# Kernel optimization log

Measured on AMD Instinct MI355X. Metric: run time of the kernel, lower is better.

Reference implementation:

```python
import jax, jax.numpy as jnp
import numpy as np

B, D, H, NS = 64, 2048, 4096, 25  # batch, x_dim (num_links), n_hidden=2*x_dim, n_steps


def setup_inputs() -> dict:
    key = jax.random.key(0)
    ks = jax.random.split(key, 12)
    # binary half-masks per leapfrog step (faithful to _construct_masks with np_seed=1)
    rng = np.random.RandomState(1)
    masks = np.zeros((NS, D), np.float32)
    for i in range(NS):
        idx = rng.permutation(D)[: D // 2]
        masks[i, idx] = 1.0
    # sinusoidal time encoding per step (_construct_time)
    ts = np.stack([
        [np.cos(2 * np.pi * i / NS), np.sin(2 * np.pi * i / NS)] for i in range(NS)
    ]).astype(np.float32)

    def lin(k, shape, fan_in):
        return jax.random.normal(k, shape, jnp.float32) / np.sqrt(fan_in)

    return dict(
        position=jax.random.normal(ks[0], (B, D), jnp.float32),
        momentum_f=jax.random.normal(ks[1], (B, D), jnp.float32),
        momentum_b=jax.random.normal(ks[2], (B, D), jnp.float32),
        u_dir=jax.random.uniform(ks[3], (B,), jnp.float32),
        u_accept=jax.random.uniform(ks[4], (B,), jnp.float32),
        eps=jnp.full((1,), 0.1, jnp.float32),
        masks=jnp.asarray(masks),
        ts=jnp.asarray(ts),
        # stacked params for the two GenericNets: [0]=position_fn, [1]=momentum_fn
        W1=lin(ks[5], (2, D, H), D), W2=lin(ks[6], (2, D, H), D),
        Wt=lin(ks[7], (2, 2, H), 2), b1=jnp.zeros((2, H), jnp.float32),
        Wh=lin(ks[8], (2, H, H), H), bh=jnp.zeros((2, H), jnp.float32),
        Ws=lin(ks[9], (2, H, D), H), bs=jnp.zeros((2, D), jnp.float32),
        cs=jnp.zeros((2, D), jnp.float32),
        Wtr=lin(ks[10], (2, H, D), H), btr=jnp.zeros((2, D), jnp.float32),
        Wq=lin(ks[11], (2, H, D), H), bq=jnp.zeros((2, D), jnp.float32),
        cq=jnp.zeros((2, D), jnp.float32),
    )


def reference(position, momentum_f, momentum_b, u_dir, u_accept, eps, masks, ts,
              W1, W2, Wt, b1, Wh, bh, Ws, bs, cs, Wtr, btr, Wq, bq, cq):
    e = eps[0]
    POS, MOM = 0, 1

    def net(n, a, b, t):
        # GenericNet: two-hidden-layer MLP emitting (scale S, translation T, transformation Q)
        h = jax.nn.relu(a @ W1[n] + b @ W2[n] + t @ Wt[n] + b1[n])
        h = jax.nn.relu(h @ Wh[n] + bh[n])
        S = jnp.tanh(h @ Ws[n] + bs[n]) * jnp.exp(cs[n])
        T = h @ Wtr[n] + btr[n]
        Q = jnp.tanh(h @ Wq[n] + bq[n]) * jnp.exp(cq[n])
        return S, T, Q

    def potential(x):              # U(1) gauge-style action: sum(1 - cos(x))
        return jnp.sum(1.0 - jnp.cos(x), axis=1)

    def grad_potential(x):
        return jnp.sin(x)

    def hamiltonian(x, v):
        return potential(x) + 0.5 * jnp.sum(v * v, axis=1)

    def mom_fwd(pos, mom, t):
        g = grad_potential(pos)
        S, T, Q = net(MOM, pos, g, t)
        sc, tr = 0.5 * e * S, e * Q
        mom = mom * jnp.exp(sc) - 0.5 * e * (jnp.exp(tr) * g - T)
        return mom, jnp.sum(sc, axis=1)

    def pos_fwd(pos, mom, t, m, minv):
        S, T, Q = net(POS, mom, m * pos, t)
        sc, tr = e * S, e * Q
        pos = m * pos + minv * (pos * jnp.exp(sc) + e * (jnp.exp(tr) * mom + T))
        return pos, jnp.sum(minv * sc, axis=1)

    def mom_bwd(pos, mom, t):
        g = grad_potential(pos)
        S, T, Q = net(MOM, pos, g, t)
        sc, tr = -0.5 * e * S, e * Q
        mom = jnp.exp(sc) * (mom + 0.5 * e * (jnp.exp(tr) * g - T))
        return mom, jnp.sum(sc, axis=1)

    def pos_bwd(pos, mom, t, m, minv):
        S, T, Q = net(POS, mom, m * pos, t)
        sc, tr = e * S, e * Q
        pos = m * pos + minv * jnp.exp(sc) * (pos - e * (jnp.exp(tr) * mom + T))
        return pos, jnp.sum(minv * sc, axis=1)

    def step_fwd(carry, xs):
        pos, mom, sld = carry
        m, t = xs
        t = t[None, :]
        minv = 1.0 - m
        mom, ld = mom_fwd(pos, mom, t); sld = sld + ld
        pos, ld = pos_fwd(pos, mom, t, m, minv); sld = sld + ld
        pos, ld = pos_fwd(pos, mom, t, minv, m); sld = sld + ld
        mom, ld = mom_fwd(pos, mom, t); sld = sld + ld
        return (pos, mom, sld), None

    def step_bwd(carry, xs):
        pos, mom, sld = carry
        m, t = xs
        t = t[None, :]
        minv = 1.0 - m
        mom, ld = mom_bwd(pos, mom, t); sld = sld + ld
        pos, ld = pos_bwd(pos, mom, t, minv, m); sld = sld + ld
        pos, ld = pos_bwd(pos, mom, t, m, minv); sld = sld + ld
        mom, ld = mom_bwd(pos, mom, t); sld = sld + ld
        return (pos, mom, sld), None

    zero = jnp.zeros(position.shape[0], position.dtype)
    (pf, mf, sldf), _ = jax.lax.scan(step_fwd, (position, momentum_f, zero), (masks, ts))
    (pb, mb, sldb), _ = jax.lax.scan(step_bwd, (position, momentum_b, zero), (masks[::-1], ts[::-1]))

    def accept_prob(mom0, pos1, mom1, sld):
        d = hamiltonian(position, mom0) - hamiltonian(pos1, mom1) + sld
        p = jnp.exp(jnp.minimum(d, 0.0))
        return jnp.where(jnp.isfinite(p), p, jnp.zeros_like(p))

    apf = accept_prob(momentum_f, pf, mf, sldf)
    apb = accept_prob(momentum_b, pb, mb, sldb)

    fmask = (u_dir > 0.5).astype(position.dtype)
    bmask = 1.0 - fmask
    position_post = fmask[:, None] * pf + bmask[:, None] * pb
    momentum_post = fmask[:, None] * mf + bmask[:, None] * mb
    ap = fmask * apf + bmask * apb
    amask = (ap > u_accept).astype(position.dtype)
    position_out = amask[:, None] * position_post + (1.0 - amask)[:, None] * position
    return position_post, momentum_post, ap, position_out
```

## Files before the change

### kernel.cpp

```cpp
#include <hip/hip_runtime.h>

#define BD   64
#define DD   2048
#define HH   4096
#define NSS  25
#define BBr  128

typedef _Float16 halfx8 __attribute__((ext_vector_type(8)));
typedef float    floatx4 __attribute__((ext_vector_type(4)));

__device__ __forceinline__ unsigned short f2h_bits(float x) {
    union { _Float16 h; unsigned short u; } c;
    c.h = (_Float16)x;
    return c.u;
}

__global__ void init_kernel(const float* __restrict__ position,
                            const float* __restrict__ momf,
                            const float* __restrict__ momb,
                            float* __restrict__ pos, float* __restrict__ mom,
                            float* __restrict__ sld,
                            unsigned short* __restrict__ Abuf) {
    int idx = blockIdx.x * 256 + threadIdx.x;
    int r = idx >> 11, d = idx & 2047;
    float p = position[((r & 63) << 11) + d];
    pos[idx] = p;
    mom[idx] = (r < 64) ? momf[(r << 11) + d] : momb[((r - 64) << 11) + d];
    Abuf[(r << 12) + d]        = f2h_bits(p);
    Abuf[(r << 12) + 2048 + d] = f2h_bits(sinf(p));
    if (idx < BBr) sld[idx] = 0.f;
}

__global__ __launch_bounds__(256) void transpose_cvt_kernel(
        const float* __restrict__ src, int ldi,
        unsigned short* __restrict__ dst, int ldo) {
    __shared__ float tile[32][33];
    const int rb = blockIdx.y * 32;
    const int cb = blockIdx.x * 32;
    const int t  = threadIdx.x;
    const int r  = t >> 3;
    const int c4 = (t & 7) * 4;
    float4 v = *reinterpret_cast<const float4*>(src + (size_t)(rb + r) * ldi + cb + c4);
    tile[r][c4 + 0] = v.x; tile[r][c4 + 1] = v.y;
    tile[r][c4 + 2] = v.z; tile[r][c4 + 3] = v.w;
    __syncthreads();
    union { unsigned short us[4]; uint2 v; } pk;
#pragma unroll
    for (int j = 0; j < 4; ++j) pk.us[j] = f2h_bits(tile[c4 + j][r]);
    *reinterpret_cast<uint2*>(dst + (size_t)(cb + r) * ldo + rb + c4) = pk.v;
}

template <int EPI>
__global__ __launch_bounds__(256) void gemm_bt_kernel(
        const unsigned short* __restrict__ A, int lda, int K,
        const unsigned short* __restrict__ BT,
        void* __restrict__ Cout, int ldc,
        const float* __restrict__ biasp, const float* __restrict__ Wtn,
        const float* __restrict__ ts, int sF, int sB) {
    const int lane = threadIdx.x & 63;
    const int wave = threadIdx.x >> 6;
    const int fl   = lane & 15;
    const int qd   = lane >> 4;
    const int bn   = blockIdx.x * 16;

    const unsigned short* pa0 = A  + (size_t)(wave * 32 + fl) * lda + qd * 8;
    const unsigned short* pa1 = pa0 + (size_t)16 * lda;
    const unsigned short* pb  = BT + (size_t)(bn + fl) * K + qd * 8;

    floatx4 acc0 = {0.f, 0.f, 0.f, 0.f};
    floatx4 acc1 = {0.f, 0.f, 0.f, 0.f};

    for (int k0 = 0; k0 < K; k0 += 128) {
#pragma unroll
        for (int u = 0; u < 4; ++u) {
            halfx8 a0 = *reinterpret_cast<const halfx8*>(pa0 + u * 32);
            halfx8 a1 = *reinterpret_cast<const halfx8*>(pa1 + u * 32);
            halfx8 b  = *reinterpret_cast<const halfx8*>(pb  + u * 32);
            acc0 = __builtin_amdgcn_mfma_f32_16x16x32_f16(a0, b, acc0, 0, 0, 0);
            acc1 = __builtin_amdgcn_mfma_f32_16x16x32_f16(a1, b, acc1, 0, 0, 0);
        }
        pa0 += 128; pa1 += 128; pb += 128;
    }

    const int col = bn + fl;
#pragma unroll
    for (int fn = 0; fn < 2; ++fn) {
        floatx4 a = (fn == 0) ? acc0 : acc1;
        const int row_base = wave * 32 + fn * 16 + qd * 4;
#pragma unroll
        for (int rr = 0; rr < 4; ++rr) {
            int row = row_base + rr;
            float v = a[rr];
            if (EPI == 0) {
                int sidx = (row < 64) ? sF : sB;
                v += biasp[col] + ts[2 * sidx] * Wtn[col] + ts[2 * sidx + 1] * Wtn[HH + col];
                v = fmaxf(v, 0.f);
                ((unsigned short*)Cout)[(size_t)row * ldc + col] = f2h_bits(v);
            } else if (EPI == 1) {
                v = fmaxf(v + biasp[col], 0.f);
                ((unsigned short*)Cout)[(size_t)row * ldc + col] = f2h_bits(v);
            } else {
                ((float*)Cout)[(size_t)row * ldc + col] = v;
            }
        }
    }
}

template <int BMODE, int EPI>
__global__ __launch_bounds__(256) void gemm_kernel(
        const unsigned short* __restrict__ A, int lda, int K,
        const float* __restrict__ Bp0, const float* __restrict__ Bp1,
        const float* __restrict__ Bp2, int ldb,
        void* __restrict__ Cout, int ldc,
        const float* __restrict__ biasp, const float* __restrict__ Wtn,
        const float* __restrict__ ts, int sF, int sB) {
    __shared__ unsigned short As[32][40];
    __shared__ unsigned short Bs[64][40];

    const int tid  = threadIdx.x;
    const int wave = tid >> 6;
    const int lane = tid & 63;
    const int fl   = lane & 15;
    const int qd   = lane >> 4;
    const int bm   = blockIdx.y * 32;
    const int bn   = blockIdx.x * 64;
    const int wm   = (wave >> 1) * 16;
    const int wn   = (wave & 1) * 32;

    const int ar = tid >> 3;
    const int ak = (tid & 7) * 4;
    const int kloc = wave * 8;
    const int bnl  = lane;

    floatx4 acc0 = {0.f, 0.f, 0.f, 0.f};
    floatx4 acc1 = {0.f, 0.f, 0.f, 0.f};

    for (int k0 = 0; k0 < K; k0 += 32) {
        *reinterpret_cast<uint2*>(&As[ar][ak]) =
            *reinterpret_cast<const uint2*>(A + (size_t)(bm + ar) * lda + k0 + ak);

        float fv[8];
        if (BMODE == 0) {
            int kk = k0 + kloc;
            const float* base = (kk < 2048) ? (Bp0 + (size_t)kk * ldb)
                                            : (Bp1 + (size_t)(kk - 2048) * ldb);
            base += bn + bnl;
#pragma unroll
            for (int j = 0; j < 8; ++j) fv[j] = base[(size_t)j * ldb];
        } else if (BMODE == 1) {
            const float* base = Bp0 + (size_t)(k0 + kloc) * ldb + bn + bnl;
#pragma unroll
            for (int j = 0; j < 8; ++j) fv[j] = base[(size_t)j * ldb];
        } else {
            int third = bn >> 11;
            const float* Bsel = (third == 0) ? Bp0 : ((third == 1) ? Bp1 : Bp2);
            const float* base = Bsel + (size_t)(k0 + kloc) * ldb + (bn - (third << 11)) + bnl;
#pragma unroll
            for (int j = 0; j < 8; ++j) fv[j] = base[(size_t)j * ldb];
        }
        union { unsigned short us[8]; uint4 v; } pk;
#pragma unroll
        for (int j = 0; j < 8; ++j) pk.us[j] = f2h_bits(fv[j]);
        *reinterpret_cast<uint4*>(&Bs[bnl][kloc]) = pk.v;

        __syncthreads();

        halfx8 afr = *reinterpret_cast<const halfx8*>(&As[wm + fl][qd * 8]);
        halfx8 bf0 = *reinterpret_cast<const halfx8*>(&Bs[wn + fl][qd * 8]);
        halfx8 bf1 = *reinterpret_cast<const halfx8*>(&Bs[wn + 16 + fl][qd * 8]);
        acc0 = __builtin_amdgcn_mfma_f32_16x16x32_f16(afr, bf0, acc0, 0, 0, 0);
        acc1 = __builtin_amdgcn_mfma_f32_16x16x32_f16(afr, bf1, acc1, 0, 0, 0);

        __syncthreads();
    }

    const int row0 = bm + wm + qd * 4;
#pragma unroll
    for (int fn = 0; fn < 2; ++fn) {
        floatx4 a = (fn == 0) ? acc0 : acc1;
        int col = bn + wn + fn * 16 + fl;
#pragma unroll
        for (int rr = 0; rr < 4; ++rr) {
            int row = row0 + rr;
            float v = a[rr];
            if (EPI == 0) {
                int sidx = (row < 64) ? sF : sB;
                v += biasp[col] + ts[2 * sidx] * Wtn[col] + ts[2 * sidx + 1] * Wtn[HH + col];
                v = fmaxf(v, 0.f);
                ((unsigned short*)Cout)[(size_t)row * ldc + col] = f2h_bits(v);
            } else if (EPI == 1) {
                v = fmaxf(v + biasp[col], 0.f);
                ((unsigned short*)Cout)[(size_t)row * ldc + col] = f2h_bits(v);
            } else {
                ((float*)Cout)[(size_t)row * ldc + col] = v;
            }
        }
    }
}

__device__ __forceinline__ void block_reduce_atomic(float v, float* dst) {
    for (int off = 32; off; off >>= 1) v += __shfl_down(v, off, 64);
    __shared__ float red[4];
    if ((threadIdx.x & 63) == 0) red[threadIdx.x >> 6] = v;
    __syncthreads();
    if (threadIdx.x == 0) atomicAdd(dst, red[0] + red[1] + red[2] + red[3]);
}

__global__ void update_mom_kernel(const float* __restrict__ pos, float* __restrict__ mom,
                                  float* __restrict__ sld, const float* __restrict__ STQ,
                                  const float* __restrict__ bs, const float* __restrict__ cs,
                                  const float* __restrict__ btr, const float* __restrict__ bq,
                                  const float* __restrict__ cq, const float* __restrict__ eps,
                                  const float* __restrict__ masks, int sF, int sB,
                                  int writeNext, unsigned short* __restrict__ Abuf) {
    int r = blockIdx.y;
    int d = blockIdx.x * 256 + threadIdx.x;
    float e = eps[0];
    size_t ro = (size_t)r * 6144;
    float S = tanhf(STQ[ro + d] + bs[d]) * expf(cs[d]);
    float T = STQ[ro + 2048 + d] + btr[d];
    float Q = tanhf(STQ[ro + 4096 + d] + bq[d]) * expf(cq[d]);
    size_t idx = (size_t)r * 2048 + d;
    float p = pos[idx], v = mom[idx];
    float g = sinf(p);
    float tr = e * Q, sc;
    if (r < 64) { sc = 0.5f * e * S;  v = v * expf(sc) - 0.5f * e * (expf(tr) * g - T); }
    else        { sc = -0.5f * e * S; v = expf(sc) * (v + 0.5f * e * (expf(tr) * g - T)); }
    mom[idx] = v;
    if (writeNext) {
        float m2 = (r < 64) ? masks[sF * 2048 + d] : 1.f - masks[sB * 2048 + d];
        Abuf[(r << 12) + d]        = f2h_bits(v);
        Abuf[(r << 12) + 2048 + d] = f2h_bits(m2 * p);
    }
    block_reduce_atomic(sc, sld + r);
}

__global__ void update_pos_kernel(float* __restrict__ pos, const float* __restrict__ mom,
                                  float* __restrict__ sld, const float* __restrict__ STQ,
                                  const float* __restrict__ bs, const float* __restrict__ cs,
                                  const float* __restrict__ btr, const float* __restrict__ bq,
                                  const float* __restrict__ cq, const float* __restrict__ eps,
                                  const float* __restrict__ masks, int sF, int sB, int sub,
                                  unsigned short* __restrict__ Abuf) {
    int r = blockIdx.y;
    int d = blockIdx.x * 256 + threadIdx.x;
    float e = eps[0];
    size_t ro = (size_t)r * 6144;
    float S = tanhf(STQ[ro + d] + bs[d]) * expf(cs[d]);
    float T = STQ[ro + 2048 + d] + btr[d];
    float Q = tanhf(STQ[ro + 4096 + d] + bq[d]) * expf(cq[d]);
    size_t idx = (size_t)r * 2048 + d;
    float p = pos[idx], v = mom[idx];
    float sc = e * S, tr = e * Q;
    float mf = masks[sF * 2048 + d], mb = masks[sB * 2048 + d];
    float pn, ld;
    if (r < 64) {
        float m  = (sub == 2) ? mf : 1.f - mf;
        float mi = 1.f - m;
        pn = m * p + mi * (p * expf(sc) + e * (expf(tr) * v + T));
        ld = mi * sc;
    } else {
        float m  = (sub == 2) ? 1.f - mb : mb;
        float mi = 1.f - m;
        pn = m * p + mi * expf(sc) * (p - e * (expf(tr) * v + T));
        ld = mi * sc;
    }
    pos[idx] = pn;
    if (sub == 2) {
        float m3 = (r < 64) ? 1.f - mf : mb;
        Abuf[(r << 12) + d]        = f2h_bits(v);
        Abuf[(r << 12) + 2048 + d] = f2h_bits(m3 * pn);
    } else {
        Abuf[(r << 12) + d]        = f2h_bits(pn);
        Abuf[(r << 12) + 2048 + d] = f2h_bits(sinf(pn));
    }
    block_reduce_atomic(ld, sld + r);
}

__global__ void accept_kernel(const float* __restrict__ position,
                              const float* __restrict__ momf, const float* __restrict__ momb,
                              const float* __restrict__ pos, const float* __restrict__ mom,
                              const float* __restrict__ sld, float* __restrict__ ap_all) {
    int r = blockIdx.x;
    int rb = r & 63;
    const float* m0 = (r < 64) ? (momf + (size_t)rb * 2048) : (momb + (size_t)rb * 2048);
    float s = 0.f;
    for (int d = threadIdx.x; d < 2048; d += 256) {
        float x0 = position[rb * 2048 + d];
        float v0 = m0[d];
        float x1 = pos[(size_t)r * 2048 + d];
        float v1 = mom[(size_t)r * 2048 + d];
        s += (cosf(x1) - cosf(x0)) + 0.5f * (v0 * v0 - v1 * v1);
    }
    for (int off = 32; off; off >>= 1) s += __shfl_down(s, off, 64);
    __shared__ float red[4];
    if ((threadIdx.x & 63) == 0) red[threadIdx.x >> 6] = s;
    __syncthreads();
    if (threadIdx.x == 0) {
        float dd = red[0] + red[1] + red[2] + red[3] + sld[r];
        float p = isnan(dd) ? 0.f : expf(dd < 0.f ? dd : 0.f);
        if (!isfinite(p)) p = 0.f;
        ap_all[r] = p;
    }
}

__global__ void combine_kernel(const float* __restrict__ position,
                               const float* __restrict__ u_dir, const float* __restrict__ u_accept,
                               const float* __restrict__ pos, const float* __restrict__ mom,
                               const float* __restrict__ ap_all, float* __restrict__ out) {
    int idx = blockIdx.x * 256 + threadIdx.x;
    int b = idx >> 11, d = idx & 2047;
    float fm = (u_dir[b] > 0.5f) ? 1.f : 0.f;
    float pf = pos[(size_t)b * 2048 + d],       pb = pos[(size_t)(64 + b) * 2048 + d];
    float mf = mom[(size_t)b * 2048 + d],       mb = mom[(size_t)(64 + b) * 2048 + d];
    float ppost = fm * pf + (1.f - fm) * pb;
    float mpost = fm * mf + (1.f - fm) * mb;
    float ap = fm * ap_all[b] + (1.f - fm) * ap_all[64 + b];
    float am = (ap > u_accept[b]) ? 1.f : 0.f;
    out[idx] = ppost;
    out[131072 + idx] = mpost;
    if (d == 0) out[262144 + b] = ap;
    out[262208 + idx] = am * ppost + (1.f - am) * position[idx];
}

extern "C" void kernel_launch(void* const* d_in, const int* in_sizes, int n_in,
                              void* d_out, int out_size, void* d_ws, size_t ws_size,
                              hipStream_t stream) {
    const float* position   = (const float*)d_in[0];
    const float* momentum_f = (const float*)d_in[1];
    const float* momentum_b = (const float*)d_in[2];
    const float* u_dir      = (const float*)d_in[3];
    const float* u_accept   = (const float*)d_in[4];
    const float* eps        = (const float*)d_in[5];
    const float* masks      = (const float*)d_in[6];
    const float* ts         = (const float*)d_in[7];
    const float* W1         = (const float*)d_in[8];
    const float* W2         = (const float*)d_in[9];
    const float* Wt         = (const float*)d_in[10];
    const float* b1         = (const float*)d_in[11];
    const float* Wh         = (const float*)d_in[12];
    const float* bh         = (const float*)d_in[13];
    const float* Ws         = (const float*)d_in[14];
    const float* bs         = (const float*)d_in[15];
    const float* cs         = (const float*)d_in[16];
    const float* Wtr        = (const float*)d_in[17];
    const float* btr        = (const float*)d_in[18];
    const float* Wq         = (const float*)d_in[19];
    const float* bq         = (const float*)d_in[20];
    const float* cq         = (const float*)d_in[21];
    float* out = (float*)d_out;

    float* pos    = (float*)d_ws;
    float* mom    = pos + BBr * DD;
    float* sld    = mom + BBr * DD;
    float* ap_all = sld + BBr;
    float* STQ    = ap_all + BBr;
    unsigned short* Abuf = (unsigned short*)(STQ + BBr * 3 * DD);
    unsigned short* h1   = Abuf + (size_t)BBr * 2 * DD;
    unsigned short* h2   = h1 + (size_t)BBr * HH;
    unsigned short* BTw  = h2 + (size_t)BBr * HH;

    const size_t BT1sz = (size_t)HH * 2 * DD;
    const size_t BThsz = (size_t)HH * HH;
    const size_t BT3sz = (size_t)3 * DD * HH;
    const size_t perNet = BT1sz + BThsz + BT3sz;
    unsigned short* BT1[2] = { BTw,                 BTw + perNet };
    unsigned short* BTh[2] = { BTw + BT1sz,         BTw + perNet + BT1sz };
    unsigned short* BT3[2] = { BTw + BT1sz + BThsz, BTw + perNet + BT1sz + BThsz };

    const size_t NEED = (size_t)((char*)(BTw + 2 * perNet) - (char*)d_ws);
    const bool fast = (ws_size >= NEED);

    const size_t DH  = (size_t)DD * HH;
    const size_t HH2 = (size_t)HH * HH;

    init_kernel<<<BBr * DD / 256, 256, 0, stream>>>(position, momentum_f, momentum_b,
                                                    pos, mom, sld, Abuf);

    if (fast) {
        for (int n = 0; n < 2; ++n) {
            transpose_cvt_kernel<<<dim3(HH / 32, DD / 32), 256, 0, stream>>>(
                W1 + n * DH, HH, BT1[n], 2 * DD);
            transpose_cvt_kernel<<<dim3(HH / 32, DD / 32), 256, 0, stream>>>(
                W2 + n * DH, HH, BT1[n] + DD, 2 * DD);
            transpose_cvt_kernel<<<dim3(HH / 32, HH / 32), 256, 0, stream>>>(
                Wh + n * HH2, HH, BTh[n], HH);
            transpose_cvt_kernel<<<dim3(DD / 32, HH / 32), 256, 0, stream>>>(
                Ws + n * DH, DD, BT3[n], HH);
            transpose_cvt_kernel<<<dim3(DD / 32, HH / 32), 256, 0, stream>>>(
                Wtr + n * DH, DD, BT3[n] + (size_t)DD * HH, HH);
            transpose_cvt_kernel<<<dim3(DD / 32, HH / 32), 256, 0, stream>>>(
                Wq + n * DH, DD, BT3[n] + (size_t)2 * DD * HH, HH);
        }
    }

    for (int i = 0; i < NSS; ++i) {
        int sF = i, sB = NSS - 1 - i;
        for (int subidx = 0; subidx < 4; ++subidx) {
            bool isMom = (subidx == 0 || subidx == 3);
            int n = isMom ? 1 : 0;
            int sub = (subidx == 1) ? 2 : 3;

            if (fast) {
                gemm_bt_kernel<0><<<HH / 16, 256, 0, stream>>>(
                    Abuf, 2 * DD, 2 * DD, BT1[n], h1, HH,
                    b1 + n * HH, Wt + n * 2 * HH, ts, sF, sB);
                gemm_bt_kernel<1><<<HH / 16, 256, 0, stream>>>(
                    h1, HH, HH, BTh[n], h2, HH,
                    bh + n * HH, nullptr, ts, sF, sB);
                gemm_bt_kernel<2><<<3 * DD / 16, 256, 0, stream>>>(
                    h2, HH, HH, BT3[n], STQ, 3 * DD,
                    nullptr, nullptr, ts, sF, sB);
            } else {
                gemm_kernel<0, 0><<<dim3(HH / 64, 4), 256, 0, stream>>>(
                    Abuf, 2 * DD, 2 * DD,
                    W1 + n * DH, W2 + n * DH, nullptr, HH, h1, HH,
                    b1 + n * HH, Wt + n * 2 * HH, ts, sF, sB);
                gemm_kernel<1, 1><<<dim3(HH / 64, 4), 256, 0, stream>>>(
                    h1, HH, HH, Wh + n * HH2, nullptr, nullptr, HH, h2, HH,
                    bh + n * HH, nullptr, ts, sF, sB);
                gemm_kernel<2, 2><<<dim3(3 * DD / 64, 4), 256, 0, stream>>>(
                    h2, HH, HH, Ws + n * DH, Wtr + n * DH, Wq + n * DH, DD, STQ, 3 * DD,
                    nullptr, nullptr, ts, sF, sB);
            }

            if (isMom)
                update_mom_kernel<<<dim3(DD / 256, BBr), 256, 0, stream>>>(
                    pos, mom, sld, STQ, bs + DD, cs + DD, btr + DD, bq + DD, cq + DD,
                    eps, masks, sF, sB, (subidx == 0) ? 1 : 0, Abuf);
            else
                update_pos_kernel<<<dim3(DD / 256, BBr), 256, 0, stream>>>(
                    pos, mom, sld, STQ, bs, cs, btr, bq, cq, eps, masks, sF, sB, sub, Abuf);
        }
    }

    accept_kernel<<<BBr, 256, 0, stream>>>(position, momentum_f, momentum_b,
                                           pos, mom, sld, ap_all);
    combine_kernel<<<BD * DD / 256, 256, 0, stream>>>(position, u_dir, u_accept,
                                                      pos, mom, ap_all, out);
}
```

Measured before the change: 19.96 ms.

## Add split-K GEMM with atomic-counter last-block reduction and fused epilogue

Adds a split-K MFMA GEMM kernel that splits K into 8 slices across blockIdx.y, computes 128x64 output tiles, and writes fp32 partials to a workspace. The last block to arrive, tracked by a per-tile atomic counter, sums the partials and applies the bias/time/ReLU or plain-store epilogue. The aim is more blocks in flight for these small-M GEMMs, which are bound by weight bandwidth, and wider N tiles that reuse A. The cost is extra partial-sum traffic, a large counter array cleared at init, and a larger workspace requirement, with a fallback to the old path when the workspace is too small.

```diff
diff --git a/kernel.cpp b/kernel.cpp
--- a/kernel.cpp
+++ b/kernel.cpp
@@ -5,6 +5,8 @@
 #define HH   4096
 #define NSS  25
 #define BBr  128
+#define SPLITK 8
+#define MAXNT  96
 
 typedef _Float16 halfx8 __attribute__((ext_vector_type(8)));
 typedef float    floatx4 __attribute__((ext_vector_type(4)));
@@ -20,7 +22,8 @@
                             const float* __restrict__ momb,
                             float* __restrict__ pos, float* __restrict__ mom,
                             float* __restrict__ sld,
-                            unsigned short* __restrict__ Abuf) {
+                            unsigned short* __restrict__ Abuf,
+                            int* __restrict__ cnt, int ncnt) {
     int idx = blockIdx.x * 256 + threadIdx.x;
     int r = idx >> 11, d = idx & 2047;
     float p = position[((r & 63) << 11) + d];
@@ -29,6 +32,7 @@
     Abuf[(r << 12) + d]        = f2h_bits(p);
     Abuf[(r << 12) + 2048 + d] = f2h_bits(sinf(p));
     if (idx < BBr) sld[idx] = 0.f;
+    if (idx < ncnt) cnt[idx] = 0;
 }
 
 __global__ __launch_bounds__(256) void transpose_cvt_kernel(
@@ -48,6 +52,107 @@
 #pragma unroll
     for (int j = 0; j < 4; ++j) pk.us[j] = f2h_bits(tile[c4 + j][r]);
     *reinterpret_cast<uint2*>(dst + (size_t)(cb + r) * ldo + rb + c4) = pk.v;
+}
+
+template <int EPI>
+__global__ __launch_bounds__(256) void gemm_splitk_kernel(
+        const unsigned short* __restrict__ A, int lda, int Kslice,
+        const unsigned short* __restrict__ BT, int ldb,
+        float* __restrict__ part, int* __restrict__ cnt,
+        void* __restrict__ Cout, int ldc,
+        const float* __restrict__ biasp, const float* __restrict__ Wtn,
+        const float* __restrict__ ts, int sF, int sB) {
+    const int nt   = blockIdx.x;
+    const int s    = blockIdx.y;
+    const int S    = (int)gridDim.y;
+    const int wave = threadIdx.x >> 6;
+    const int lane = threadIdx.x & 63;
+    const int fl   = lane & 15;
+    const int qd   = lane >> 4;
+    const int bn   = nt * 64;
+    const int k0   = s * Kslice;
+
+    const unsigned short* pa = A  + (size_t)(wave * 32 + fl) * lda + k0 + qd * 8;
+    const unsigned short* pb = BT + (size_t)(bn + fl) * ldb + k0 + qd * 8;
+    const size_t la16 = (size_t)16 * lda;
+    const size_t lb16 = (size_t)16 * ldb;
+
+    floatx4 acc[2][4];
+#pragma unroll
+    for (int i = 0; i < 2; ++i)
+#pragma unroll
+        for (int j = 0; j < 4; ++j) acc[i][j] = (floatx4){0.f, 0.f, 0.f, 0.f};
+
+    for (int k = 0; k < Kslice; k += 64) {
+#pragma unroll
+        for (int u = 0; u < 2; ++u) {
+            halfx8 a0 = *reinterpret_cast<const halfx8*>(pa + u * 32);
+            halfx8 a1 = *reinterpret_cast<const halfx8*>(pa + la16 + u * 32);
+            halfx8 b0 = *reinterpret_cast<const halfx8*>(pb + u * 32);
+            halfx8 b1 = *reinterpret_cast<const halfx8*>(pb + lb16 + u * 32);
+            halfx8 b2 = *reinterpret_cast<const halfx8*>(pb + 2 * lb16 + u * 32);
+            halfx8 b3 = *reinterpret_cast<const halfx8*>(pb + 3 * lb16 + u * 32);
+            acc[0][0] = __builtin_amdgcn_mfma_f32_16x16x32_f16(a0, b0, acc[0][0], 0, 0, 0);
+            acc[0][1] = __builtin_amdgcn_mfma_f32_16x16x32_f16(a0, b1, acc[0][1], 0, 0, 0);
+            acc[0][2] = __builtin_amdgcn_mfma_f32_16x16x32_f16(a0, b2, acc[0][2], 0, 0, 0);
+            acc[0][3] = __builtin_amdgcn_mfma_f32_16x16x32_f16(a0, b3, acc[0][3], 0, 0, 0);
+            acc[1][0] = __builtin_amdgcn_mfma_f32_16x16x32_f16(a1, b0, acc[1][0], 0, 0, 0);
+            acc[1][1] = __builtin_amdgcn_mfma_f32_16x16x32_f16(a1, b1, acc[1][1], 0, 0, 0);
+            acc[1][2] = __builtin_amdgcn_mfma_f32_16x16x32_f16(a1, b2, acc[1][2], 0, 0, 0);
+            acc[1][3] = __builtin_amdgcn_mfma_f32_16x16x32_f16(a1, b3, acc[1][3], 0, 0, 0);
+        }
+        pa += 64; pb += 64;
+    }
+
+    float* pt = part + (size_t)(nt * S + s) * 8192;
+#pragma unroll
+    for (int fn = 0; fn < 2; ++fn)
+#pragma unroll
+        for (int j = 0; j < 4; ++j)
+#pragma unroll
+            for (int rr = 0; rr < 4; ++rr) {
+                int row = wave * 32 + fn * 16 + qd * 4 + rr;
+                int col = j * 16 + fl;
+                pt[row * 64 + col] = acc[fn][j][rr];
+            }
+
+    __threadfence();
+    __syncthreads();
+    __shared__ int oldc;
+    if (threadIdx.x == 0) oldc = atomicAdd(cnt + nt, 1);
+    __syncthreads();
+    if (oldc != S - 1) return;
+    __threadfence();
+
+    const float* basep = part + (size_t)nt * S * 8192;
+    for (int e0 = threadIdx.x * 4; e0 < 8192; e0 += 1024) {
+        float vx = 0.f, vy = 0.f, vz = 0.f, vw = 0.f;
+        for (int ss = 0; ss < S; ++ss) {
+            float4 p = *reinterpret_cast<const float4*>(basep + (size_t)ss * 8192 + e0);
+            vx += p.x; vy += p.y; vz += p.z; vw += p.w;
+        }
+        int row = e0 >> 6;
+        int col = bn + (e0 & 63);
+        if (EPI == 2) {
+            float4 o = {vx, vy, vz, vw};
+            *reinterpret_cast<float4*>((float*)Cout + (size_t)row * ldc + col) = o;
+        } else {
+            float v4[4] = {vx, vy, vz, vw};
+            union { unsigned short us[4]; uint2 u2; } pk;
+            float t0 = 0.f, t1 = 0.f;
+            if (EPI == 0) {
+                int sidx = (row < 64) ? sF : sB;
+                t0 = ts[2 * sidx]; t1 = ts[2 * sidx + 1];
+            }
+#pragma unroll
+            for (int q = 0; q < 4; ++q) {
+                float x = v4[q] + biasp[col + q];
+                if (EPI == 0) x += t0 * Wtn[col + q] + t1 * Wtn[HH + col + q];
+                pk.us[q] = f2h_bits(fmaxf(x, 0.f));
+            }
+            *reinterpret_cast<uint2*>((unsigned short*)Cout + (size_t)row * ldc + col) = pk.u2;
+        }
+    }
 }
 
 template <int EPI>
@@ -368,16 +473,23 @@
     unsigned short* BTh[2] = { BTw + BT1sz,         BTw + perNet + BT1sz };
     unsigned short* BT3[2] = { BTw + BT1sz + BThsz, BTw + perNet + BT1sz + BThsz };
 
-    const size_t NEED = (size_t)((char*)(BTw + 2 * perNet) - (char*)d_ws);
-    const bool fast = (ws_size >= NEED);
+    int* cnt = (int*)(BTw + 2 * perNet);
+    const int NCNT = 300 * MAXNT;
+    float* part = (float*)(cnt + NCNT);
+
+    const size_t NEED_MID  = (size_t)((char*)cnt - (char*)d_ws);
+    const size_t NEED_FULL = (size_t)((char*)(part + (size_t)MAXNT * SPLITK * 8192) - (char*)d_ws);
+    const bool haveW  = (ws_size >= NEED_MID);
+    const bool fastSK = (ws_size >= NEED_FULL);
 
     const size_t DH  = (size_t)DD * HH;
     const size_t HH2 = (size_t)HH * HH;
 
     init_kernel<<<BBr * DD / 256, 256, 0, stream>>>(position, momentum_f, momentum_b,
-                                                    pos, mom, sld, Abuf);
-
-    if (fast) {
+                                                    pos, mom, sld, Abuf,
+                                                    fastSK ? cnt : (int*)sld, fastSK ? NCNT : 0);
+
+    if (haveW) {
         for (int n = 0; n < 2; ++n) {
             transpose_cvt_kernel<<<dim3(HH / 32, DD / 32), 256, 0, stream>>>(
                 W1 + n * DH, HH, BT1[n], 2 * DD);
@@ -394,14 +506,30 @@
         }
     }
 
+    const int KS = HH / SPLITK;
+
     for (int i = 0; i < NSS; ++i) {
         int sF = i, sB = NSS - 1 - i;
         for (int subidx = 0; subidx < 4; ++subidx) {
             bool isMom = (subidx == 0 || subidx == 3);
             int n = isMom ? 1 : 0;
             int sub = (subidx == 1) ? 2 : 3;
-
-            if (fast) {
+            int step = i * 4 + subidx;
+
+            if (fastSK) {
+                gemm_splitk_kernel<0><<<dim3(HH / 64, SPLITK), 256, 0, stream>>>(
+                    Abuf, 2 * DD, KS, BT1[n], 2 * DD,
+                    part, cnt + (step * 3 + 0) * MAXNT, h1, HH,
+                    b1 + n * HH, Wt + n * 2 * HH, ts, sF, sB);
+                gemm_splitk_kernel<1><<<dim3(HH / 64, SPLITK), 256, 0, stream>>>(
+                    h1, HH, KS, BTh[n], HH,
+                    part, cnt + (step * 3 + 1) * MAXNT, h2, HH,
+                    bh + n * HH, nullptr, ts, sF, sB);
+                gemm_splitk_kernel<2><<<dim3(3 * DD / 64, SPLITK), 256, 0, stream>>>(
+                    h2, HH, KS, BT3[n], HH,
+                    part, cnt + (step * 3 + 2) * MAXNT, STQ, 3 * DD,
+                    nullptr, nullptr, ts, sF, sB);
+            } else if (haveW) {
                 gemm_bt_kernel<0><<<HH / 16, 256, 0, stream>>>(
                     Abuf, 2 * DD, 2 * DD, BT1[n], h1, HH,
                     b1 + n * HH, Wt + n * 2 * HH, ts, sF, sB);
```

After: 37.01 ms. 85.4% more time.
